# Performance work log

Measured on AMD Instinct MI355X. Metric: run time of the kernel, lower is better.

## Reference

```python
import jax, jax.numpy as jnp
import numpy as np

B, NL, NH, NG, NC, GOI = 1024, 64, 32, 20000, 64, 1000
EPS = 1e-5


def setup_inputs() -> dict:
    key = jax.random.key(0)
    ks = jax.random.split(key, 8)
    latent = jax.random.normal(ks[0], (B, NL), dtype=jnp.float32)
    genes_oi = jax.random.randint(ks[1], (GOI,), 0, NG, dtype=jnp.int64)
    W = jax.random.normal(ks[2], (NL, NH), dtype=jnp.float32) / np.sqrt(NL)
    b = jnp.zeros((NH,), dtype=jnp.float32)
    bn_gamma = jnp.ones((NH,), dtype=jnp.float32)
    bn_beta = jnp.zeros((NH,), dtype=jnp.float32)
    bn_mean = jnp.zeros((NH,), dtype=jnp.float32)
    bn_var = jnp.ones((NH,), dtype=jnp.float32)
    logit_table = jax.random.normal(ks[3], (NG, NH, NC), dtype=jnp.float32) * 0.02
    rho_table = jax.random.uniform(ks[4], (NG, NH), dtype=jnp.float32,
                                   minval=-1.0 / np.sqrt(NH), maxval=1.0 / np.sqrt(NH))
    return {"latent": latent, "genes_oi": genes_oi, "W": W, "b": b,
            "bn_gamma": bn_gamma, "bn_beta": bn_beta, "bn_mean": bn_mean,
            "bn_var": bn_var, "logit_table": logit_table, "rho_table": rho_table}


def reference(latent, genes_oi, W, b, bn_gamma, bn_beta, bn_mean, bn_var,
              logit_table, rho_table):
    # MLP: Linear -> BatchNorm1d (eval, running stats) -> ReLU (dropout off in eval)
    h = latent @ W + b                                      # [B, NH]
    h = (h - bn_mean) * jax.lax.rsqrt(bn_var + EPS) * bn_gamma + bn_beta
    h = jax.nn.relu(h)
    # sparse gather of per-gene weight tensors, then batched small matmul
    lw = logit_table[genes_oi]                              # [GOI, NH, NC]
    logit = jnp.einsum('bh,ghc->bgc', h, lw)                # [B, GOI, NC]
    rho = h @ rho_table.T                                   # [B, NG] (full weight)
    return (logit, rho)
```

## Files before the change

kernel.cpp:

```cpp
#include <hip/hip_runtime.h>

#define BATCH 1024
#define NL    64
#define NH    32
#define NG    20000
#define NC    64
#define GOI   1000

#define LOGIT_BLOCKS (GOI * 4)
#define RHO_NGRP     ((NG + 63) / 64)
#define RHO_YB       (BATCH / 64)
#define RHO_BLOCKS   (RHO_NGRP * RHO_YB)

typedef __attribute__((ext_vector_type(8))) short  short8;
typedef __attribute__((ext_vector_type(4))) float  f32x4;

static __device__ __forceinline__ unsigned short f2bf(float f) {
    unsigned int u = __builtin_bit_cast(unsigned int, f);
    unsigned int r = (u + 0x7fffu + ((u >> 16) & 1u)) >> 16;
    return (unsigned short)r;
}

__global__ __launch_bounds__(256) void h_kernel(
    const float* __restrict__ latent,
    const float* __restrict__ W,
    const float* __restrict__ bias,
    const float* __restrict__ gamma,
    const float* __restrict__ beta,
    const float* __restrict__ mean,
    const float* __restrict__ var,
    unsigned short* __restrict__ h)
{
    int tid = blockIdx.x * 256 + threadIdx.x;
    int b = tid >> 5;
    int k = tid & 31;
    float acc = 0.f;
    #pragma unroll 8
    for (int j = 0; j < NL; ++j)
        acc += latent[b * NL + j] * W[j * NH + k];
    acc += bias[k];
    float x = (acc - mean[k]) * rsqrtf(var[k] + 1e-5f) * gamma[k] + beta[k];
    x = fmaxf(x, 0.f);
    h[tid] = f2bf(x);
}

__global__ __launch_bounds__(256) void main_kernel(
    const unsigned short* __restrict__ h,
    const float*          __restrict__ ltab,
    const int*            __restrict__ genes,
    const float*          __restrict__ rtab,
    float*                __restrict__ out_logit,
    float*                __restrict__ out_rho)
{
    const int wave = threadIdx.x >> 6;
    const int lane = threadIdx.x & 63;
    const int l15  = lane & 15;
    const int quad = lane >> 4;
    const int bx   = blockIdx.x;

    if (bx < LOGIT_BLOCKS) {
        const int g   = bx >> 2;
        const int ybl = bx & 3;

        const long long gene = (long long)genes[g];
        const float* lw = ltab + gene * (long long)(NH * NC);

        short8 bf[4];
        #pragma unroll
        for (int t = 0; t < 4; ++t) {
            #pragma unroll
            for (int j = 0; j < 8; ++j)
                bf[t][j] = (short)f2bf(lw[(quad * 8 + j) * NC + t * 16 + l15]);
        }

        #pragma unroll
        for (int it = 0; it < 4; ++it) {
            const int b0 = ybl * 256 + it * 64 + wave * 16;
            short8 af = *(const short8*)(h + (b0 + l15) * NH + quad * 8);

            f32x4 acc[4];
            #pragma unroll
            for (int t = 0; t < 4; ++t) {
                f32x4 z = {0.f, 0.f, 0.f, 0.f};
                acc[t] = __builtin_amdgcn_mfma_f32_16x16x32_bf16(bf[t], af, z, 0, 0, 0);
            }

            float* op = out_logit +
                ((long long)(b0 + l15) * GOI + g) * NC + quad * 4;
            #pragma unroll
            for (int t = 0; t < 4; ++t)
                *(f32x4*)(op + t * 16) = acc[t];
        }
    } else {
        const int rb = bx - LOGIT_BLOCKS;
        const int yb = rb & 15;
        const int ng = rb >> 4;
        const int b0 = yb * 64 + wave * 16;

        short8 af = *(const short8*)(h + (b0 + l15) * NH + quad * 8);

        #pragma unroll
        for (int t = 0; t < 4; ++t) {
            const int n0 = ng * 64 + t * 16;
            if (n0 < NG) {
                const float* rp = rtab + (long long)(n0 + l15) * NH + quad * 8;
                short8 bfr;
                #pragma unroll
                for (int j = 0; j < 8; ++j)
                    bfr[j] = (short)f2bf(rp[j]);
                f32x4 z = {0.f, 0.f, 0.f, 0.f};
                f32x4 acc = __builtin_amdgcn_mfma_f32_16x16x32_bf16(bfr, af, z, 0, 0, 0);
                float* op = out_rho +
                    (long long)(b0 + l15) * NG + n0 + quad * 4;
                *(f32x4*)op = acc;
            }
        }
    }
}

extern "C" void kernel_launch(void* const* d_in, const int* in_sizes, int n_in,
                              void* d_out, int out_size, void* d_ws, size_t ws_size,
                              hipStream_t stream) {
    const float* latent = (const float*)d_in[0];
    const int*   genes  = (const int*)d_in[1];
    const float* W      = (const float*)d_in[2];
    const float* bias   = (const float*)d_in[3];
    const float* gamma  = (const float*)d_in[4];
    const float* beta   = (const float*)d_in[5];
    const float* mean   = (const float*)d_in[6];
    const float* var    = (const float*)d_in[7];
    const float* ltab   = (const float*)d_in[8];
    const float* rtab   = (const float*)d_in[9];

    float* out = (float*)d_out;
    unsigned short* h = (unsigned short*)d_ws;

    float* out_logit = out;
    float* out_rho   = out + (long long)BATCH * GOI * NC;

    h_kernel<<<dim3((BATCH * NH) / 256), 256, 0, stream>>>(
        latent, W, bias, gamma, beta, mean, var, h);

    main_kernel<<<dim3(LOGIT_BLOCKS + RHO_BLOCKS), 256, 0, stream>>>(
        h, ltab, genes, rtab, out_logit, out_rho);
}
```

Measured before the change: 476.7 us.

## Fuse MLP into main kernel and make blocks loop over gene slices

Merges the hidden-layer kernel into the main kernel: each block recomputes the bf16 hidden activations for its 64 batch rows in shared memory. Blocks become persistent-style workers, 16 row groups by 64 slices, each iterating over a range of genes and rho column groups. This removes a kernel launch and the workspace round trip. The trade-off is fewer blocks and less occupancy for latency hiding, plus redundant MLP recomputation per slice.

```diff
diff --git a/kernel.cpp b/kernel.cpp
--- a/kernel.cpp
+++ b/kernel.cpp
@@ -7,10 +7,10 @@
 #define NC    64
 #define GOI   1000
 
-#define LOGIT_BLOCKS (GOI * 4)
-#define RHO_NGRP     ((NG + 63) / 64)
-#define RHO_YB       (BATCH / 64)
-#define RHO_BLOCKS   (RHO_NGRP * RHO_YB)
+#define NGRP   313
+#define RGS    16
+#define SLICES 64
+#define NBLK   (RGS * SLICES)
 
 typedef __attribute__((ext_vector_type(8))) short  short8;
 typedef __attribute__((ext_vector_type(4))) float  f32x4;
@@ -21,7 +21,7 @@
     return (unsigned short)r;
 }
 
-__global__ __launch_bounds__(256) void h_kernel(
+__global__ __launch_bounds__(256) void fused_kernel(
     const float* __restrict__ latent,
     const float* __restrict__ W,
     const float* __restrict__ bias,
@@ -29,42 +29,70 @@
     const float* __restrict__ beta,
     const float* __restrict__ mean,
     const float* __restrict__ var,
-    unsigned short* __restrict__ h)
+    const float* __restrict__ ltab,
+    const int*   __restrict__ genes,
+    const float* __restrict__ rtab,
+    float*       __restrict__ out_logit,
+    float*       __restrict__ out_rho)
 {
-    int tid = blockIdx.x * 256 + threadIdx.x;
-    int b = tid >> 5;
-    int k = tid & 31;
-    float acc = 0.f;
-    #pragma unroll 8
-    for (int j = 0; j < NL; ++j)
-        acc += latent[b * NL + j] * W[j * NH + k];
-    acc += bias[k];
-    float x = (acc - mean[k]) * rsqrtf(var[k] + 1e-5f) * gamma[k] + beta[k];
-    x = fmaxf(x, 0.f);
-    h[tid] = f2bf(x);
-}
+    __shared__ float          Wl[NL * NH];
+    __shared__ unsigned short hl[64 * NH];
 
-__global__ __launch_bounds__(256) void main_kernel(
-    const unsigned short* __restrict__ h,
-    const float*          __restrict__ ltab,
-    const int*            __restrict__ genes,
-    const float*          __restrict__ rtab,
-    float*                __restrict__ out_logit,
-    float*                __restrict__ out_rho)
-{
-    const int wave = threadIdx.x >> 6;
-    const int lane = threadIdx.x & 63;
+    const int tid = threadIdx.x;
+    const int bid = blockIdx.x;
+    const int rg  = bid & (RGS - 1);
+    const int s   = bid >> 4;
+    const int r0  = rg * 64;
+
+    {
+        f32x4*       dst = (f32x4*)Wl;
+        const f32x4* src = (const f32x4*)W;
+        dst[tid * 2]     = src[tid * 2];
+        dst[tid * 2 + 1] = src[tid * 2 + 1];
+    }
+    __syncthreads();
+
+    {
+        const int lrow = tid >> 2;
+        const int k0   = (tid & 3) * 8;
+        const float* lp = latent + (long long)(r0 + lrow) * NL;
+        float acc[8] = {0.f,0.f,0.f,0.f,0.f,0.f,0.f,0.f};
+        #pragma unroll
+        for (int jb = 0; jb < NL / 4; ++jb) {
+            const f32x4 l4 = *(const f32x4*)(lp + jb * 4);
+            #pragma unroll
+            for (int i = 0; i < 4; ++i) {
+                const int j = jb * 4 + i;
+                #pragma unroll
+                for (int jj = 0; jj < 8; ++jj)
+                    acc[jj] += l4[i] * Wl[j * NH + k0 + jj];
+            }
+        }
+        short8 pack;
+        #pragma unroll
+        for (int jj = 0; jj < 8; ++jj) {
+            const int k = k0 + jj;
+            float x = acc[jj] + bias[k];
+            x = (x - mean[k]) * rsqrtf(var[k] + 1e-5f) * gamma[k] + beta[k];
+            pack[jj] = (short)f2bf(fmaxf(x, 0.f));
+        }
+        *(short8*)&hl[lrow * NH + k0] = pack;
+    }
+    __syncthreads();
+
+    const int wave = tid >> 6;
+    const int lane = tid & 63;
     const int l15  = lane & 15;
     const int quad = lane >> 4;
-    const int bx   = blockIdx.x;
 
-    if (bx < LOGIT_BLOCKS) {
-        const int g   = bx >> 2;
-        const int ybl = bx & 3;
+    const short8 af = *(const short8*)&hl[(wave * 16 + l15) * NH + quad * 8];
+    const long long brow = (long long)(r0 + wave * 16 + l15);
 
+    const int g0 = (s * GOI) >> 6;
+    const int g1 = ((s + 1) * GOI) >> 6;
+    for (int g = g0; g < g1; ++g) {
         const long long gene = (long long)genes[g];
         const float* lw = ltab + gene * (long long)(NH * NC);
-
         short8 bf[4];
         #pragma unroll
         for (int t = 0; t < 4; ++t) {
@@ -72,33 +100,18 @@
             for (int j = 0; j < 8; ++j)
                 bf[t][j] = (short)f2bf(lw[(quad * 8 + j) * NC + t * 16 + l15]);
         }
+        float* op = out_logit + (brow * GOI + g) * NC + quad * 4;
+        #pragma unroll
+        for (int t = 0; t < 4; ++t) {
+            f32x4 z = {0.f, 0.f, 0.f, 0.f};
+            f32x4 acc = __builtin_amdgcn_mfma_f32_16x16x32_bf16(bf[t], af, z, 0, 0, 0);
+            *(f32x4*)(op + t * 16) = acc;
+        }
+    }
 
-        #pragma unroll
-        for (int it = 0; it < 4; ++it) {
-            const int b0 = ybl * 256 + it * 64 + wave * 16;
-            short8 af = *(const short8*)(h + (b0 + l15) * NH + quad * 8);
-
-            f32x4 acc[4];
-            #pragma unroll
-            for (int t = 0; t < 4; ++t) {
-                f32x4 z = {0.f, 0.f, 0.f, 0.f};
-                acc[t] = __builtin_amdgcn_mfma_f32_16x16x32_bf16(bf[t], af, z, 0, 0, 0);
-            }
-
-            float* op = out_logit +
-                ((long long)(b0 + l15) * GOI + g) * NC + quad * 4;
-            #pragma unroll
-            for (int t = 0; t < 4; ++t)
-                *(f32x4*)(op + t * 16) = acc[t];
-        }
-    } else {
-        const int rb = bx - LOGIT_BLOCKS;
-        const int yb = rb & 15;
-        const int ng = rb >> 4;
-        const int b0 = yb * 64 + wave * 16;
-
-        short8 af = *(const short8*)(h + (b0 + l15) * NH + quad * 8);
-
+    const int n0g = (s * NGRP) >> 6;
+    const int n1g = ((s + 1) * NGRP) >> 6;
+    for (int ng = n0g; ng < n1g; ++ng) {
         #pragma unroll
         for (int t = 0; t < 4; ++t) {
             const int n0 = ng * 64 + t * 16;
@@ -110,9 +123,7 @@
                     bfr[j] = (short)f2bf(rp[j]);
                 f32x4 z = {0.f, 0.f, 0.f, 0.f};
                 f32x4 acc = __builtin_amdgcn_mfma_f32_16x16x32_bf16(bfr, af, z, 0, 0, 0);
-                float* op = out_rho +
-                    (long long)(b0 + l15) * NG + n0 + quad * 4;
-                *(f32x4*)op = acc;
+                *(f32x4*)(out_rho + brow * NG + n0 + quad * 4) = acc;
             }
         }
     }
@@ -133,14 +144,10 @@
     const float* rtab   = (const float*)d_in[9];
 
     float* out = (float*)d_out;
-    unsigned short* h = (unsigned short*)d_ws;
-
     float* out_logit = out;
     float* out_rho   = out + (long long)BATCH * GOI * NC;
 
-    h_kernel<<<dim3((BATCH * NH) / 256), 256, 0, stream>>>(
-        latent, W, bias, gamma, beta, mean, var, h);
-
-    main_kernel<<<dim3(LOGIT_BLOCKS + RHO_BLOCKS), 256, 0, stream>>>(
-        h, ltab, genes, rtab, out_logit, out_rho);
+    fused_kernel<<<dim3(NBLK), 256, 0, stream>>>(
+        latent, W, bias, gamma, beta, mean, var,
+        ltab, genes, rtab, out_logit, out_rho);
 }
```

After: 529.5 us. +11.1%, slower.
